# Performance work log

Measured on AMD Instinct MI355X. Metric: run time of the kernel, lower is better.

The kernel has to match this reference:

```python
import jax, jax.numpy as jnp
import numpy as np

B, K, MAX_PER = 128, 3, 48
MAX_TOK = MAX_PER * K  # 144 decode steps
LATENT, HDIM, NMEM = 128, 512, 8
NHEADS, VOCAB = 8, 8000
DH = HDIM // NHEADS
BOS, EOS = 1, 2
ACTIVE_THRESH = 0.01


def setup_inputs() -> dict:
    key = jax.random.key(0)
    ks = jax.random.split(key, 15)
    w = lambda i, sh: jax.random.normal(ks[i], sh, jnp.float32) * 0.05
    return {
        'z_seq': jax.random.normal(ks[0], (B, K, LATENT), jnp.float32),
        'z_weights': jax.random.uniform(ks[1], (B, K), dtype=jnp.float32),
        'W_l2d': w(2, (LATENT, NMEM * HDIM)),
        'token_emb': w(3, (VOCAB, HDIM)),
        'Wq': w(4, (HDIM, HDIM)), 'Wk': w(5, (HDIM, HDIM)),
        'Wv': w(6, (HDIM, HDIM)), 'Wo': w(7, (HDIM, HDIM)),
        'Wcq': w(8, (HDIM, HDIM)), 'Wck': w(9, (HDIM, HDIM)),
        'Wcv': w(10, (HDIM, HDIM)), 'Wco': w(11, (HDIM, HDIM)),
        'W1': w(12, (HDIM, 4 * HDIM)), 'W2': w(13, (4 * HDIM, HDIM)),
        'Wout': w(14, (HDIM, VOCAB)),
    }


def _forward(z_seq, z_weights, W_l2d, token_emb, Wq, Wk, Wv, Wo,
             Wcq, Wck, Wcv, Wco, W1, W2, Wout):
    scale = float(1.0 / np.sqrt(DH))
    ab = jnp.arange(B)
    # weighted_z = z_weights.unsqueeze(-1) * z_seq; memories via latent_to_decoder
    weighted_z = z_weights[..., None] * z_seq                     # [B,K,L]
    memories = (weighted_z.reshape(B * K, LATENT) @ W_l2d).reshape(B, K, NMEM, HDIM)
    active = z_weights > ACTIVE_THRESH                            # [B,K]

    def gated_mem(cur_phr, done):
        i = jnp.minimum(cur_phr, K - 1)
        m = memories[ab, i]                                       # [B,NMEM,HDIM]
        gate = (active[ab, i] & ~done).astype(m.dtype)
        return m * gate[:, None, None]

    def attn_step(x, m, kc, vc, step):
        # x: [B,HDIM] current token hidden; m: gated memories [B,NMEM,HDIM]
        q = (x @ Wq).reshape(B, NHEADS, DH)
        k = (x @ Wk).reshape(B, 1, NHEADS, DH)
        v = (x @ Wv).reshape(B, 1, NHEADS, DH)
        kc = jax.lax.dynamic_update_slice(kc, k, (0, step, 0, 0))
        vc = jax.lax.dynamic_update_slice(vc, v, (0, step, 0, 0))
        s = jnp.einsum('bhd,bthd->bht', q, kc) * scale
        tmask = jnp.arange(MAX_TOK + 1) <= step                   # valid cache slots
        s = jnp.where(tmask[None, None, :], s, -1e30)
        sa = jnp.einsum('bht,bthd->bhd', jax.nn.softmax(s, axis=-1), vc).reshape(B, HDIM)
        x = x + sa @ Wo
        cq = (x @ Wcq).reshape(B, NHEADS, DH)
        ck = (m @ Wck).reshape(B, NMEM, NHEADS, DH)
        cv = (m @ Wcv).reshape(B, NMEM, NHEADS, DH)
        cs = jnp.einsum('bhd,bmhd->bhm', cq, ck) * scale
        ca = jnp.einsum('bhm,bmhd->bhd', jax.nn.softmax(cs, axis=-1), cv).reshape(B, HDIM)
        x = x + ca @ Wco
        x = x + jax.nn.gelu(x @ W1) @ W2
        return x, kc, vc

    kc = jnp.zeros((B, MAX_TOK + 1, NHEADS, DH), jnp.float32)
    vc = jnp.zeros_like(kc)
    done = ~active[:, 0]
    cur_phr = jnp.zeros(B, jnp.int32)
    tip = jnp.zeros(B, jnp.int32)   # tok_in_phr
    pos = jnp.zeros(B, jnp.int32)
    tokens = jnp.zeros((B, MAX_TOK), jnp.int32)
    genm = jnp.zeros((B, MAX_TOK), bool)
    bounds = jnp.zeros((B, K), jnp.int32)
    emb0 = jnp.broadcast_to(token_emb[BOS], (B, HDIM))
    out, kc, vc = attn_step(emb0, gated_mem(cur_phr, done), kc, vc, 0)

    def body(carry, t):
        out, kc, vc, tokens, genm, bounds, cur_phr, tip, pos, done = carry
        logits = out @ Wout
        nxt = jnp.argmax(logits, axis=-1).astype(jnp.int32)
        live = ~done
        tokens = tokens.at[ab, pos].set(jnp.where(live, nxt, 0))
        genm = genm.at[ab, pos].set(live)
        pos = pos + live.astype(jnp.int32)
        tip = tip + live.astype(jnp.int32)
        eos = (nxt == EOS) & (tip >= 1)
        switch = (eos | (tip >= MAX_PER)) & live
        cur_phr = cur_phr + switch.astype(jnp.int32)
        tip = tip * (~switch).astype(jnp.int32)
        sv = switch & (cur_phr < K)
        cp = jnp.minimum(cur_phr, K - 1)
        bounds = bounds.at[ab, cp].set(jnp.where(sv, pos, bounds[ab, cp]))
        done = done | (cur_phr >= K) | (switch & ~active[ab, cp])
        new_out, kc, vc = attn_step(token_emb[nxt], gated_mem(cur_phr, done), kc, vc, t + 1)
        return (new_out, kc, vc, tokens, genm, bounds, cur_phr, tip, pos, done), out

    carry = (out, kc, vc, tokens, genm, bounds, cur_phr, tip, pos, done)
    carry, hiddens = jax.lax.scan(body, carry, jnp.arange(MAX_TOK))
    # tokens, gen_mask, bounds (as in torch _decode) plus per-step hiddens [T,B,H]
    return carry[3], carry[4], carry[5], hiddens


def reference(z_seq, z_weights, W_l2d, token_emb, Wq, Wk, Wv, Wo, Wcq, Wck, Wcv, Wco, W1, W2, Wout):
    return _forward(z_seq, z_weights, W_l2d, token_emb, Wq, Wk, Wv, Wo,
                    Wcq, Wck, Wcv, Wco, W1, W2, Wout)
```

## Files before the change

kernel.cpp:

```cpp
#include <hip/hip_runtime.h>
#include <math.h>

#define NB 128
#define KPH 3
#define MAXPER 48
#define MAXTOK 144
#define LATENT 128
#define HD 512
#define NMEM 8
#define NH 8
#define VOC 8000
#define CT 145
#define NBLK 512
#define SCALE 0.125f

__device__ __forceinline__ float ldsc(const float* p) {
  return __hip_atomic_load(const_cast<float*>(p), __ATOMIC_RELAXED, __HIP_MEMORY_SCOPE_AGENT);
}
__device__ __forceinline__ void stsc(float* p, float v) {
  __hip_atomic_store(p, v, __ATOMIC_RELAXED, __HIP_MEMORY_SCOPE_AGENT);
}
__device__ __forceinline__ int ldsci(const int* p) {
  return __hip_atomic_load(const_cast<int*>(p), __ATOMIC_RELAXED, __HIP_MEMORY_SCOPE_AGENT);
}
__device__ __forceinline__ void stsci(int* p, int v) {
  __hip_atomic_store(p, v, __ATOMIC_RELAXED, __HIP_MEMORY_SCOPE_AGENT);
}

__device__ __forceinline__ void gload_lds(const float* g, float* l) {
  __builtin_amdgcn_global_load_lds(
      (const __attribute__((address_space(1))) unsigned int*)g,
      (__attribute__((address_space(3))) unsigned int*)l, 4, 0, 0);
}


__global__ void k_zero(float* __restrict__ p, int n) {
  int i = blockIdx.x * blockDim.x + threadIdx.x;
  if (i < n) p[i] = 0.0f;
}

__global__ void k_wz(const float* __restrict__ z_seq, const float* __restrict__ zw,
                     float* __restrict__ out) {
  int i = blockIdx.x * blockDim.x + threadIdx.x;
  if (i < NB * KPH * LATENT) out[i] = zw[i >> 7] * z_seq[i];
}

__global__ void k_copy(const float* __restrict__ src, float* __restrict__ dst, int n) {
  int i = blockIdx.x * blockDim.x + threadIdx.x;
  if (i < n) dst[i] = src[i];
}

__global__ __launch_bounds__(256) void k_gemm(
    const float* __restrict__ A, int lda,
    const float* __restrict__ W, int ldw, int K,
    float* __restrict__ out, int ostride)
{
  __shared__ float As[32][36];
  __shared__ float Ws[32][64];
  const int t = threadIdx.x;
  const int c0 = blockIdx.x * 64, b0 = blockIdx.y * 32;
  const int c = t & 63, g = t >> 6;
  float acc[8] = {0,0,0,0,0,0,0,0};
  const int ra = t >> 3, ka = (t & 7) << 2;
  for (int k0 = 0; k0 < K; k0 += 32) {
    const float4 a4 = *reinterpret_cast<const float4*>(A + (size_t)(b0 + ra) * lda + k0 + ka);
    As[ra][ka] = a4.x; As[ra][ka+1] = a4.y; As[ra][ka+2] = a4.z; As[ra][ka+3] = a4.w;
    #pragma unroll
    for (int e = 0; e < 8; e++) {
      int li = t + e * 256;
      Ws[li >> 6][li & 63] = W[(size_t)(k0 + (li >> 6)) * ldw + c0 + (li & 63)];
    }
    __syncthreads();
    #pragma unroll
    for (int kk = 0; kk < 32; kk++) {
      float wv = Ws[kk][c];
      #pragma unroll
      for (int i = 0; i < 8; i++) acc[i] += As[g*8+i][kk] * wv;
    }
    __syncthreads();
  }
  #pragma unroll
  for (int i = 0; i < 8; i++)
    out[(size_t)(b0 + g * 8 + i) * ostride + c0 + c] = acc[i];
}

__global__ void k_init(const float* __restrict__ zw,
                       int* __restrict__ cur, int* __restrict__ tip, int* __restrict__ pos,
                       int* __restrict__ done, float* __restrict__ gf, int* __restrict__ iph,
                       int* __restrict__ nxt0, int* __restrict__ act)
{
  int b = blockIdx.x * blockDim.x + threadIdx.x;
  if (b < NB) {
    int a0 = zw[b*3+0] > 0.01f;
    act[b*3+0] = a0;
    act[b*3+1] = zw[b*3+1] > 0.01f;
    act[b*3+2] = zw[b*3+2] > 0.01f;
    cur[b] = 0; tip[b] = 0; pos[b] = 0; done[b] = !a0;
    gf[b] = a0 ? 1.0f : 0.0f; iph[b] = 0;
    nxt0[b] = 1;
  }
}


struct DecP {
  const float *temb, *Wq, *Wk, *Wv, *Wo, *Wco, *W1, *W2, *Wout;
  const float *MCK, *MCV, *WCAT;
  float *KC, *VC, *XS, *X2, *X3, *X, *Qb, *CQ, *CQ2, *H1, *GP, *PV, *GF;
  int *PI, *CUR, *TIP, *POS, *DONE, *IPH, *NXT0, *ACT;
  float *TOK, *GEN, *BND, *HID;
  unsigned *bar;
};

__device__ __forceinline__ void gsync(unsigned* bar, unsigned epoch) {
  const int t = threadIdx.x, blk = blockIdx.x;
  __syncthreads();
  if (t == 0)
    __hip_atomic_fetch_add(&bar[(blk & 63) * 32], 1u,
                           __ATOMIC_RELAXED, __HIP_MEMORY_SCOPE_AGENT);
  if (blk == 0) {
    if (t < 64) {
      const unsigned tg = epoch * (NBLK / 64);
      while (__hip_atomic_load(&bar[t * 32], __ATOMIC_RELAXED, __HIP_MEMORY_SCOPE_AGENT) < tg)
        __builtin_amdgcn_s_sleep(2);
      if (t < 8)
        __hip_atomic_store(&bar[2048 + t * 32], epoch,
                           __ATOMIC_RELAXED, __HIP_MEMORY_SCOPE_AGENT);
    }
  } else if (t == 0) {
    while (__hip_atomic_load(&bar[2048 + (blk & 7) * 32],
                             __ATOMIC_RELAXED, __HIP_MEMORY_SCOPE_AGENT) < epoch)
      __builtin_amdgcn_s_sleep(8);
  }
  __syncthreads();
}

__global__ __launch_bounds__(256, 2) void k_decode(DecP p) {
  __shared__ float Ws2[2][64][64];
  __shared__ float U[8704];
  __shared__ int   snxt[8];

  const int t = threadIdx.x;
  const int blk = blockIdx.x;
  unsigned ep = 0;

  auto gemm8 = [&](int bx, int by, const float* A, int lda,
                   const float* W, int ldw, int K,
                   const float* R, int rs,
                   float* out, int os, int oo, int dogelu) {
    float (*As2)[8][72] = (float(*)[8][72])U;
    const int c0 = bx * 64, b0 = by * 8;
    const int c = t & 63, g = t >> 6;
    const int ar = t & 7, ak = t >> 3;
    const int nslab = K >> 6;
    float acc0 = 0.f, acc1 = 0.f;
    float res0 = 0.f, res1 = 0.f;
    if (R) {
      res0 = ldsc(R + (size_t)(b0 + g * 2 + 0) * rs + c0 + c);
      res1 = ldsc(R + (size_t)(b0 + g * 2 + 1) * rs + c0 + c);
    }
    float aR0 = ldsc(A + (size_t)(b0 + ar) * lda + ak);
    float aR1 = ldsc(A + (size_t)(b0 + ar) * lda + 32 + ak);
    #pragma unroll
    for (int e = 0; e < 16; e++)
      gload_lds(W + (size_t)(g * 16 + e) * ldw + c0 + c, &Ws2[0][g * 16 + e][0]);
    for (int j = 0; j < nslab; j++) {
      const int cur = j & 1;
      As2[cur][ar][ak] = aR0;
      As2[cur][ar][ak + 32] = aR1;
      __syncthreads();
      if (j + 1 < nslab) {
        aR0 = ldsc(A + (size_t)(b0 + ar) * lda + (j + 1) * 64 + ak);
        aR1 = ldsc(A + (size_t)(b0 + ar) * lda + (j + 1) * 64 + 32 + ak);
        #pragma unroll
        for (int e = 0; e < 16; e++)
          gload_lds(W + (size_t)((j + 1) * 64 + g * 16 + e) * ldw + c0 + c,
                    &Ws2[cur ^ 1][g * 16 + e][0]);
      }
      #pragma unroll
      for (int kk = 0; kk < 64; kk++) {
        float wv = Ws2[cur][kk][c];
        acc0 += As2[cur][g * 2 + 0][kk] * wv;
        acc1 += As2[cur][g * 2 + 1][kk] * wv;
      }
      __syncthreads();
    }
    #pragma unroll
    for (int i = 0; i < 2; i++) {
      float v = (i == 0) ? acc0 : acc1;
      int b = b0 + g * 2 + i;
      v += (i == 0) ? res0 : res1;
      if (dogelu) {
        float x3 = v * v * v;
        v = 0.5f * v * (1.0f + tanhf(0.7978845608028654f * (v + 0.044715f * x3)));
      }
      stsc(out + (size_t)b * os + oo + c0 + c, v);
    }
  };

  auto gemm8g = [&](int bx, int b0, const float* W,
                    float* out, int os, int oo) {
    float (*As2)[8][72] = (float(*)[8][72])U;
    const int c0 = bx * 64;
    const int c = t & 63, g = t >> 6;
    const int ar = t & 7, ak = t >> 3;
    float acc0 = 0.f, acc1 = 0.f;
    const float* Ar = p.temb + (size_t)snxt[ar] * 512;
    float aR0 = Ar[ak];
    float aR1 = Ar[32 + ak];
    #pragma unroll
    for (int e = 0; e < 16; e++)
      gload_lds(W + (size_t)(g * 16 + e) * 512 + c0 + c, &Ws2[0][g * 16 + e][0]);
    for (int j = 0; j < 8; j++) {
      const int cur = j & 1;
      As2[cur][ar][ak] = aR0;
      As2[cur][ar][ak + 32] = aR1;
      __syncthreads();
      if (j + 1 < 8) {
        aR0 = Ar[(j + 1) * 64 + ak];
        aR1 = Ar[(j + 1) * 64 + 32 + ak];
        #pragma unroll
        for (int e = 0; e < 16; e++)
          gload_lds(W + (size_t)((j + 1) * 64 + g * 16 + e) * 512 + c0 + c,
                    &Ws2[cur ^ 1][g * 16 + e][0]);
      }
      #pragma unroll
      for (int kk = 0; kk < 64; kk++) {
        float wv = Ws2[cur][kk][c];
        acc0 += As2[cur][g * 2 + 0][kk] * wv;
        acc1 += As2[cur][g * 2 + 1][kk] * wv;
      }
      __syncthreads();
    }
    #pragma unroll
    for (int i = 0; i < 2; i++) {
      float v = (i == 0) ? acc0 : acc1;
      int b = b0 + g * 2 + i;
      stsc(out + (size_t)b * os + oo + c0 + c, v);
    }
  };

  auto logits_tile = [&](int bx, int by) {
    float (*AsL)[32][72] = (float(*)[32][72])U;
    const int c0 = bx * 64, b0 = by * 32;
    const int c = t & 63, g = t >> 6;
    const int ar = t & 31, akb = (t >> 5) * 8;
    const int cg = t & 15, rg = t >> 4;
    float acc[2][4] = {{0,0,0,0},{0,0,0,0}};
    float aR[8];
    const float* Ab = p.X + (size_t)(b0 + ar) * 512 + akb;
    #pragma unroll
    for (int u = 0; u < 8; u++) aR[u] = ldsc(Ab + u);
    #pragma unroll
    for (int e = 0; e < 16; e++)
      gload_lds(p.Wout + (size_t)(g * 16 + e) * VOC + c0 + c, &Ws2[0][g * 16 + e][0]);
    for (int j = 0; j < 8; j++) {
      const int cur = j & 1;
      #pragma unroll
      for (int u = 0; u < 8; u++) AsL[cur][ar][akb + u] = aR[u];
      __syncthreads();
      if (j + 1 < 8) {
        #pragma unroll
        for (int u = 0; u < 8; u++) aR[u] = ldsc(Ab + (j + 1) * 64 + u);
        #pragma unroll
        for (int e = 0; e < 16; e++)
          gload_lds(p.Wout + (size_t)((j + 1) * 64 + g * 16 + e) * VOC + c0 + c,
                    &Ws2[cur ^ 1][g * 16 + e][0]);
      }
      #pragma unroll
      for (int kk = 0; kk < 64; kk++) {
        float4 w4 = *reinterpret_cast<const float4*>(&Ws2[cur][kk][cg * 4]);
        float a0 = AsL[cur][rg * 2 + 0][kk];
        float a1 = AsL[cur][rg * 2 + 1][kk];
        acc[0][0] += a0 * w4.x; acc[0][1] += a0 * w4.y;
        acc[0][2] += a0 * w4.z; acc[0][3] += a0 * w4.w;
        acc[1][0] += a1 * w4.x; acc[1][1] += a1 * w4.y;
        acc[1][2] += a1 * w4.z; acc[1][3] += a1 * w4.w;
      }
      __syncthreads();
    }
    #pragma unroll
    for (int i = 0; i < 2; i++) {
      float bv = acc[i][0]; int bix = c0 + cg * 4;
      #pragma unroll
      for (int u = 1; u < 4; u++) {
        float v = acc[i][u];
        if (v > bv) { bv = v; bix = c0 + cg * 4 + u; }
      }
      #pragma unroll
      for (int off = 1; off < 16; off <<= 1) {
        float v2 = __shfl_xor(bv, off, 64);
        int   i2 = __shfl_xor(bix, off, 64);
        if (v2 > bv || (v2 == bv && i2 < bix)) { bv = v2; bix = i2; }
      }
      if (cg == 0) {
        stsc(&p.PV[(size_t)(b0 + rg * 2 + i) * 125 + bx], bv);
        stsci(&p.PI[(size_t)(b0 + rg * 2 + i) * 125 + bx], bix);
      }
    }
    __syncthreads();
  };

  auto state_phase = [&](int s, int b0, int desig) {
    const int r = t >> 5, j = t & 31, b = b0 + r;
    const int vOld = (s - 1) & 1, vNew = s & 1;
    if (s > 0) {
      float bv = -INFINITY; int bix = 0x7fffffff;
      for (int i = j; i < 125; i += 32) {
        float v = ldsc(&p.PV[(size_t)b * 125 + i]);
        int  id = ldsci(&p.PI[(size_t)b * 125 + i]);
        if (v > bv || (v == bv && id < bix)) { bv = v; bix = id; }
      }
      #pragma unroll
      for (int off = 16; off; off >>= 1) {
        float v2 = __shfl_xor(bv, off, 64);
        int   i2 = __shfl_xor(bix, off, 64);
        if (v2 > bv || (v2 == bv && i2 < bix)) { bv = v2; bix = i2; }
      }
      if (j == 0) {
        int nxt = bix;
        int dn = ldsci(&p.DONE[vOld*NB+b]); int live = !dn;
        int pp = ldsci(&p.POS[vOld*NB+b]);
        int tp = ldsci(&p.TIP[vOld*NB+b]);
        int cp = ldsci(&p.CUR[vOld*NB+b]);
        if (desig && pp < MAXTOK) {
          p.TOK[(size_t)b*MAXTOK+pp] = live ? (float)nxt : 0.0f;
          p.GEN[(size_t)b*MAXTOK+pp] = live ? 1.0f : 0.0f;
        }
        pp += live; tp += live;
        int eos = (nxt == 2) && (tp >= 1);
        int sw = (eos || (tp >= MAXPER)) && live;
        cp += sw;
        if (sw) tp = 0;
        int cpc = cp < 2 ? cp : 2;
        if (desig && sw && (cp < KPH)) p.BND[(size_t)b*KPH+cpc] = (float)pp;
        dn = dn || (cp >= KPH) || (sw && !p.ACT[b*3+cpc]);
        stsci(&p.CUR[vNew*NB+b], cp);
        stsci(&p.TIP[vNew*NB+b], tp);
        stsci(&p.POS[vNew*NB+b], pp);
        stsci(&p.DONE[vNew*NB+b], dn);
        stsc(&p.GF[vNew*NB+b], (p.ACT[b*3+cpc] && !dn) ? 1.0f : 0.0f);
        stsci(&p.IPH[vNew*NB+b], cpc);
        snxt[r] = nxt;
      }
    } else {
      if (j == 0) snxt[r] = p.NXT0[b];
    }
    __syncthreads();
  };

  for (int s = 0; s < MAXTOK; s++) {
    if (blk < 384) {
      int which = blk >> 7;
      int loc = blk & 127, bx = loc & 7, by = loc >> 3;
      int b0 = by * 8;
      int desig = (which == 0 && bx == 0);
      state_phase(s, b0, desig);
      if (desig) {
        #pragma unroll
        for (int rep = 0; rep < 16; rep++) {
          int idx = t + rep * 256;
          int rr = idx >> 9, cc = idx & 511;
          stsc(&p.XS[(size_t)(b0 + rr) * 1024 + cc],
               p.temb[(size_t)snxt[rr] * 512 + cc]);
        }
      }
      if (which == 0)      gemm8g(bx, b0, p.Wq, p.Qb, 512, 0);
      else if (which == 1) gemm8g(bx, b0, p.Wk, p.KC, CT*512, s*512);
      else                 gemm8g(bx, b0, p.Wv, p.VC, CT*512, s*512);
    }
    gsync(p.bar, ++ep);

    if (blk < 256) {
      float (*aux)[224] = (float(*)[224])U;
      const int T = s + 1;
      int lane = t & 63, w = t >> 6;
      int task = blk * 4 + w, b = task >> 3, h = task & 7;
      float* ql = aux[w];
      float* sc = aux[w] + 64;
      ql[lane] = ldsc(&p.Qb[(size_t)b * 512 + h * 64 + lane]);
      __syncthreads();
      float lmax = -INFINITY;
      for (int s0 = lane; s0 < T; s0 += 64) {
        const float4* kp = reinterpret_cast<const float4*>(p.KC + ((size_t)b * CT + s0) * 512 + h * 64);
        float d = 0.0f;
        #pragma unroll
        for (int e = 0; e < 16; e++) {
          float4 k4 = kp[e];
          d += ql[4*e]*k4.x + ql[4*e+1]*k4.y + ql[4*e+2]*k4.z + ql[4*e+3]*k4.w;
        }
        d *= SCALE;
        sc[s0] = d;
        lmax = fmaxf(lmax, d);
      }
      #pragma unroll
      for (int off = 32; off; off >>= 1) lmax = fmaxf(lmax, __shfl_xor(lmax, off, 64));
      float lsum = 0.0f;
      for (int s0 = lane; s0 < T; s0 += 64) {
        float e = expf(sc[s0] - lmax);
        sc[s0] = e; lsum += e;
      }
      #pragma unroll
      for (int off = 32; off; off >>= 1) lsum += __shfl_xor(lsum, off, 64);
      __syncthreads();
      float inv = 1.0f / lsum;
      float acc = 0.0f;
      const float* vb = p.VC + (size_t)b * CT * 512 + h * 64 + lane;
      #pragma unroll 4
      for (int s0 = 0; s0 < T; s0++) acc += sc[s0] * vb[(size_t)s0 * 512];
      stsc(&p.XS[(size_t)b * 1024 + 512 + h * 64 + lane], acc * inv);
    }
    gsync(p.bar, ++ep);

    if (blk < 128)
      gemm8(blk & 7, blk >> 3, p.XS + 512, 1024, p.Wo, 512, 512, p.XS, 1024, p.X2, 512, 0, 0);
    else if (blk < 256) {
      int l = blk - 128;
      gemm8(l & 7, l >> 3, p.XS, 1024, p.WCAT, 512, 512, nullptr, 0, p.CQ, 512, 0, 0);
    } else if (blk < 384) {
      int l = blk - 256;
      gemm8(l & 7, l >> 3, p.XS + 512, 1024, p.WCAT + (size_t)512*512, 512, 512,
            nullptr, 0, p.CQ2, 512, 0, 0);
    }
    gsync(p.bar, ++ep);

    if (blk < NB) {
      const int b = blk;
      const int vNew = s & 1;
      float* cq  = U;
      float* ca  = U + 512;
      float* scs = U + 1024;
      cq[t]       = ldsc(&p.CQ[(size_t)b * 512 + t])       + ldsc(&p.CQ2[(size_t)b * 512 + t]);
      cq[t + 256] = ldsc(&p.CQ[(size_t)b * 512 + t + 256]) + ldsc(&p.CQ2[(size_t)b * 512 + t + 256]);
      __syncthreads();
      float gate = ldsc(&p.GF[vNew*NB+b]);
      int ip = ldsci(&p.IPH[vNew*NB+b]);
      const float* mk = p.MCK + (size_t)(b * KPH + ip) * NMEM * 512;
      if (t < 64) {
        int h = t >> 3, m = t & 7;
        const float4* kp = reinterpret_cast<const float4*>(mk + m * 512 + h * 64);
        float d = 0.0f;
        #pragma unroll
        for (int e = 0; e < 16; e++) {
          float4 k4 = kp[e];
          d += cq[h*64+4*e]*k4.x + cq[h*64+4*e+1]*k4.y + cq[h*64+4*e+2]*k4.z + cq[h*64+4*e+3]*k4.w;
        }
        scs[t] = d * SCALE * gate;
      }
      __syncthreads();
      const float* mv = p.MCV + (size_t)(b * KPH + ip) * NMEM * 512;
      #pragma unroll
      for (int half = 0; half < 2; half++) {
        int c = t + half * 256;
        int h = c >> 6;
        float mx = scs[h*8];
        #pragma unroll
        for (int m = 1; m < 8; m++) mx = fmaxf(mx, scs[h*8+m]);
        float ee[8]; float sum = 0.0f;
        #pragma unroll
        for (int m = 0; m < 8; m++) { ee[m] = expf(scs[h*8+m] - mx); sum += ee[m]; }
        float a = 0.0f;
        #pragma unroll
        for (int m = 0; m < 8; m++) a += ee[m] * mv[(size_t)m * 512 + c];
        ca[c] = gate * a / sum;
      }
      __syncthreads();
      #pragma unroll
      for (int half = 0; half < 2; half++) {
        int c = t + half * 256;
        float acc = 0.0f;
        const float* wc = p.Wco + c;
        #pragma unroll 8
        for (int k = 0; k < 512; k++) acc += ca[k] * wc[(size_t)k * 512];
        stsc(&p.X3[(size_t)b * 512 + c], acc + ldsc(&p.X2[(size_t)b * 512 + c]));
      }
    }
    gsync(p.bar, ++ep);

    gemm8(blk & 31, blk >> 5, p.X3, 512, p.W1, 2048, 512, nullptr, 0, p.H1, 2048, 0, 1);
    gsync(p.bar, ++ep);

    {
      int ks = blk >> 7, loc = blk & 127;
      gemm8(loc & 7, loc >> 3, p.H1 + ks * 512, 2048,
            p.W2 + (size_t)ks * 512 * 512, 512, 512,
            nullptr, 0, p.GP + (size_t)ks * NB * 512, 512, 0, 0);
    }
    gsync(p.bar, ++ep);

    if (blk < 256) {
      int el = blk * 256 + t;
      float v = ldsc(&p.X3[el])
              + ldsc(&p.GP[el]) + ldsc(&p.GP[NB*512 + el])
              + ldsc(&p.GP[2*NB*512 + el]) + ldsc(&p.GP[3*NB*512 + el]);
      stsc(&p.X[el], v);
      p.HID[(size_t)s * NB * 512 + el] = v;
    }
    gsync(p.bar, ++ep);

    {
      const int x = blk & 7, idx2 = blk >> 3;
      const int ii = idx2 & 15, by = idx2 >> 4;
      const int bx = x + 8 * ii;
      if (bx < 125) logits_tile(bx, by);
    }
    gsync(p.bar, ++ep);
  }

  if (blk < 128 && (blk & 7) == 0) {
    const int b0 = (blk >> 3) * 8;
    state_phase(MAXTOK, b0, 1);
  }
}


extern "C" void kernel_launch(void* const* d_in, const int* in_sizes, int n_in,
                              void* d_out, int out_size, void* d_ws, size_t ws_size,
                              hipStream_t stream)
{
  const float* z_seq = (const float*)d_in[0];
  const float* z_w   = (const float*)d_in[1];
  const float* W_l2d = (const float*)d_in[2];
  const float* temb  = (const float*)d_in[3];
  const float* Wq  = (const float*)d_in[4];
  const float* Wk  = (const float*)d_in[5];
  const float* Wv  = (const float*)d_in[6];
  const float* Wo  = (const float*)d_in[7];
  const float* Wcq = (const float*)d_in[8];
  const float* Wck = (const float*)d_in[9];
  const float* Wcv = (const float*)d_in[10];
  const float* Wco = (const float*)d_in[11];
  const float* W1  = (const float*)d_in[12];
  const float* W2  = (const float*)d_in[13];
  const float* Wout= (const float*)d_in[14];

  float* fw = (float*)d_ws;
  size_t o = 4096;
  auto alloc = [&](size_t n) { float* r = fw + o; o += (n + 63) & ~(size_t)63; return r; };
  float* MCK = alloc((size_t)NB*KPH*NMEM*HD);
  float* MCV = alloc((size_t)NB*KPH*NMEM*HD);
  float* MEM = alloc((size_t)NB*KPH*NMEM*HD);
  float* KC  = alloc((size_t)NB*CT*HD);
  float* VC  = alloc((size_t)NB*CT*HD);
  float* XS  = alloc((size_t)NB*1024);
  float* X2  = alloc((size_t)NB*HD);
  float* X3  = alloc((size_t)NB*HD);
  float* X   = alloc((size_t)NB*HD);
  float* Qb  = alloc((size_t)NB*HD);
  float* CQ  = alloc((size_t)NB*HD);
  float* H1  = alloc((size_t)NB*4*HD);
  float* WZ  = alloc((size_t)NB*KPH*LATENT);
  float* PV  = alloc((size_t)NB*125);
  float* GF  = alloc(2*NB);
  int* ib = (int*)alloc(0);
  size_t io = 0;
  auto ialloc = [&](size_t n) { int* r = ib + io; io += (n + 63) & ~(size_t)63; return r; };
  int* PI   = ialloc((size_t)NB*125);
  int* CUR  = ialloc(2*NB);
  int* TIP  = ialloc(2*NB);
  int* POS  = ialloc(2*NB);
  int* DONE = ialloc(2*NB);
  int* IPH  = ialloc(2*NB);
  int* NXT0 = ialloc(NB);
  int* ACT  = ialloc(NB*KPH);

  float* WCAT = MEM;
  float* GP   = MEM + (size_t)1024*512;
  float* CQ2  = GP  + (size_t)4*NB*HD;

  float* out_f = (float*)d_out;
  float* TOK  = out_f;
  float* GEN  = out_f + NB*MAXTOK;
  float* BND  = out_f + 2*NB*MAXTOK;
  float* HID  = out_f + 2*NB*MAXTOK + NB*KPH;

  k_zero<<<16, 256, 0, stream>>>(fw, 4096);
  int nz = 2*NB*MAXTOK + NB*KPH;
  k_zero<<<(nz + 255)/256, 256, 0, stream>>>(out_f, nz);
  k_wz<<<(NB*KPH*LATENT + 255)/256, 256, 0, stream>>>(z_seq, z_w, WZ);
  k_gemm<<<dim3(64,12),256,0,stream>>>(WZ, 128, W_l2d, 4096, 128, MEM, 4096);
  k_gemm<<<dim3(8,96),256,0,stream>>>(MEM, 512, Wck, 512, 512, MCK, 512);
  k_gemm<<<dim3(8,96),256,0,stream>>>(MEM, 512, Wcv, 512, 512, MCV, 512);
  k_gemm<<<dim3(8,16),256,0,stream>>>(Wo, 512, Wcq, 512, 512, WCAT + (size_t)512*512, 512);
  k_copy<<<(512*512 + 255)/256, 256, 0, stream>>>(Wcq, WCAT, 512*512);
  k_init<<<1,128,0,stream>>>(z_w, CUR, TIP, POS, DONE, GF, IPH, NXT0, ACT);

  DecP prm;
  prm.temb = temb; prm.Wq = Wq; prm.Wk = Wk; prm.Wv = Wv; prm.Wo = Wo;
  prm.Wco = Wco; prm.W1 = W1; prm.W2 = W2; prm.Wout = Wout;
  prm.MCK = MCK; prm.MCV = MCV; prm.WCAT = WCAT;
  prm.KC = KC; prm.VC = VC; prm.XS = XS; prm.X2 = X2; prm.X3 = X3; prm.X = X;
  prm.Qb = Qb; prm.CQ = CQ; prm.CQ2 = CQ2; prm.H1 = H1; prm.GP = GP;
  prm.PV = PV; prm.GF = GF;
  prm.PI = PI; prm.CUR = CUR; prm.TIP = TIP; prm.POS = POS; prm.DONE = DONE;
  prm.IPH = IPH; prm.NXT0 = NXT0; prm.ACT = ACT;
  prm.TOK = TOK; prm.GEN = GEN; prm.BND = BND; prm.HID = HID;
  prm.bar = (unsigned*)d_ws;

  k_decode<<<dim3(NBLK), dim3(256), 0, stream>>>(prm);
}
```

Measured before the change: 30.28 ms.

## Widen GEMM tiles to 128 columns and cut active blocks per phase

The persistent decode kernel's GEMM helpers now compute 128-column tiles with 2x2 register blocking over 32-wide K slabs, replacing 64-column tiles. The logits GEMM uses 128x32 tiles with 4x4 blocking, which halves the number of argmax partials per row from 125 to 63. Each phase now uses fewer blocks (192 or 256 instead of 384 or 512). The aim is more reuse per loaded weight and fewer partial results, at the cost of less parallelism per phase and more barrier steps per slab.

```diff
diff --git a/kernel.cpp b/kernel.cpp
--- a/kernel.cpp
+++ b/kernel.cpp
@@ -143,158 +143,173 @@
   const int blk = blockIdx.x;
   unsigned ep = 0;
 
-  auto gemm8 = [&](int bx, int by, const float* A, int lda,
+  const int wv = t >> 6, lc = t & 63;
+
+  auto gemm4 = [&](int bx, int by, const float* A, int lda,
                    const float* W, int ldw, int K,
                    const float* R, int rs,
                    float* out, int os, int oo, int dogelu) {
-    float (*As2)[8][72] = (float(*)[8][72])U;
-    const int c0 = bx * 64, b0 = by * 8;
-    const int c = t & 63, g = t >> 6;
-    const int ar = t & 7, ak = t >> 3;
-    const int nslab = K >> 6;
-    float acc0 = 0.f, acc1 = 0.f;
-    float res0 = 0.f, res1 = 0.f;
+    float (*Ws)[32][128] = (float(*)[32][128])Ws2;
+    float (*As)[8][36]   = (float(*)[8][36])U;
+    const int c0 = bx * 128, b0 = by * 8;
+    const int cg = t & 63, rg = t >> 6;
+    const int sr = t >> 5, sk = t & 31;
+    const int nslab = K >> 5;
+    float acc[2][2] = {{0.f,0.f},{0.f,0.f}};
+    float res[2][2] = {{0.f,0.f},{0.f,0.f}};
     if (R) {
-      res0 = ldsc(R + (size_t)(b0 + g * 2 + 0) * rs + c0 + c);
-      res1 = ldsc(R + (size_t)(b0 + g * 2 + 1) * rs + c0 + c);
-    }
-    float aR0 = ldsc(A + (size_t)(b0 + ar) * lda + ak);
-    float aR1 = ldsc(A + (size_t)(b0 + ar) * lda + 32 + ak);
+      #pragma unroll
+      for (int i = 0; i < 2; i++)
+        #pragma unroll
+        for (int jj = 0; jj < 2; jj++)
+          res[i][jj] = ldsc(R + (size_t)(b0 + rg * 2 + i) * rs + c0 + cg * 2 + jj);
+    }
+    float aS = ldsc(A + (size_t)(b0 + sr) * lda + sk);
     #pragma unroll
     for (int e = 0; e < 16; e++)
-      gload_lds(W + (size_t)(g * 16 + e) * ldw + c0 + c, &Ws2[0][g * 16 + e][0]);
+      gload_lds(W + (size_t)(wv * 8 + (e >> 1)) * ldw + c0 + (e & 1) * 64 + lc,
+                &Ws[0][wv * 8 + (e >> 1)][(e & 1) * 64]);
     for (int j = 0; j < nslab; j++) {
       const int cur = j & 1;
-      As2[cur][ar][ak] = aR0;
-      As2[cur][ar][ak + 32] = aR1;
+      As[cur][sr][sk] = aS;
       __syncthreads();
       if (j + 1 < nslab) {
-        aR0 = ldsc(A + (size_t)(b0 + ar) * lda + (j + 1) * 64 + ak);
-        aR1 = ldsc(A + (size_t)(b0 + ar) * lda + (j + 1) * 64 + 32 + ak);
+        aS = ldsc(A + (size_t)(b0 + sr) * lda + (j + 1) * 32 + sk);
         #pragma unroll
         for (int e = 0; e < 16; e++)
-          gload_lds(W + (size_t)((j + 1) * 64 + g * 16 + e) * ldw + c0 + c,
-                    &Ws2[cur ^ 1][g * 16 + e][0]);
-      }
-      #pragma unroll
-      for (int kk = 0; kk < 64; kk++) {
-        float wv = Ws2[cur][kk][c];
-        acc0 += As2[cur][g * 2 + 0][kk] * wv;
-        acc1 += As2[cur][g * 2 + 1][kk] * wv;
+          gload_lds(W + (size_t)((j + 1) * 32 + wv * 8 + (e >> 1)) * ldw + c0 + (e & 1) * 64 + lc,
+                    &Ws[cur ^ 1][wv * 8 + (e >> 1)][(e & 1) * 64]);
+      }
+      #pragma unroll
+      for (int kk = 0; kk < 32; kk++) {
+        float2 w2 = *reinterpret_cast<const float2*>(&Ws[cur][kk][cg * 2]);
+        float a0 = As[cur][rg * 2 + 0][kk];
+        float a1 = As[cur][rg * 2 + 1][kk];
+        acc[0][0] += a0 * w2.x; acc[0][1] += a0 * w2.y;
+        acc[1][0] += a1 * w2.x; acc[1][1] += a1 * w2.y;
       }
       __syncthreads();
     }
     #pragma unroll
     for (int i = 0; i < 2; i++) {
-      float v = (i == 0) ? acc0 : acc1;
-      int b = b0 + g * 2 + i;
-      v += (i == 0) ? res0 : res1;
-      if (dogelu) {
-        float x3 = v * v * v;
-        v = 0.5f * v * (1.0f + tanhf(0.7978845608028654f * (v + 0.044715f * x3)));
-      }
-      stsc(out + (size_t)b * os + oo + c0 + c, v);
+      #pragma unroll
+      for (int jj = 0; jj < 2; jj++) {
+        float v = acc[i][jj] + res[i][jj];
+        if (dogelu) {
+          float x3 = v * v * v;
+          v = 0.5f * v * (1.0f + tanhf(0.7978845608028654f * (v + 0.044715f * x3)));
+        }
+        stsc(out + (size_t)(b0 + rg * 2 + i) * os + oo + c0 + cg * 2 + jj, v);
+      }
     }
   };
 
-  auto gemm8g = [&](int bx, int b0, const float* W,
+  auto gemm4g = [&](int bx, int b0, const float* W,
                     float* out, int os, int oo) {
-    float (*As2)[8][72] = (float(*)[8][72])U;
-    const int c0 = bx * 64;
-    const int c = t & 63, g = t >> 6;
-    const int ar = t & 7, ak = t >> 3;
-    float acc0 = 0.f, acc1 = 0.f;
-    const float* Ar = p.temb + (size_t)snxt[ar] * 512;
-    float aR0 = Ar[ak];
-    float aR1 = Ar[32 + ak];
+    float (*Ws)[32][128] = (float(*)[32][128])Ws2;
+    float (*As)[8][36]   = (float(*)[8][36])U;
+    const int c0 = bx * 128;
+    const int cg = t & 63, rg = t >> 6;
+    const int sr = t >> 5, sk = t & 31;
+    float acc[2][2] = {{0.f,0.f},{0.f,0.f}};
+    const float* Ar = p.temb + (size_t)snxt[sr] * 512;
+    float aS = Ar[sk];
     #pragma unroll
     for (int e = 0; e < 16; e++)
-      gload_lds(W + (size_t)(g * 16 + e) * 512 + c0 + c, &Ws2[0][g * 16 + e][0]);
-    for (int j = 0; j < 8; j++) {
+      gload_lds(W + (size_t)(wv * 8 + (e >> 1)) * 512 + c0 + (e & 1) * 64 + lc,
+                &Ws[0][wv * 8 + (e >> 1)][(e & 1) * 64]);
+    for (int j = 0; j < 16; j++) {
       const int cur = j & 1;
-      As2[cur][ar][ak] = aR0;
-      As2[cur][ar][ak + 32] = aR1;
-      __syncthreads();
-      if (j + 1 < 8) {
-        aR0 = Ar[(j + 1) * 64 + ak];
-        aR1 = Ar[(j + 1) * 64 + 32 + ak];
+      As[cur][sr][sk] = aS;
+      __syncthreads();
+      if (j + 1 < 16) {
+        aS = Ar[(j + 1) * 32 + sk];
         #pragma unroll
         for (int e = 0; e < 16; e++)
-          gload_lds(W + (size_t)((j + 1) * 64 + g * 16 + e) * 512 + c0 + c,
-                    &Ws2[cur ^ 1][g * 16 + e][0]);
-      }
-      #pragma unroll
-      for (int kk = 0; kk < 64; kk++) {
-        float wv = Ws2[cur][kk][c];
-        acc0 += As2[cur][g * 2 + 0][kk] * wv;
-        acc1 += As2[cur][g * 2 + 1][kk] * wv;
-      }
-      __syncthreads();
-    }
-    #pragma unroll
-    for (int i = 0; i < 2; i++) {
-      float v = (i == 0) ? acc0 : acc1;
-      int b = b0 + g * 2 + i;
-      stsc(out + (size_t)b * os + oo + c0 + c, v);
-    }
+          gload_lds(W + (size_t)((j + 1) * 32 + wv * 8 + (e >> 1)) * 512 + c0 + (e & 1) * 64 + lc,
+                    &Ws[cur ^ 1][wv * 8 + (e >> 1)][(e & 1) * 64]);
+      }
+      #pragma unroll
+      for (int kk = 0; kk < 32; kk++) {
+        float2 w2 = *reinterpret_cast<const float2*>(&Ws[cur][kk][cg * 2]);
+        float a0 = As[cur][rg * 2 + 0][kk];
+        float a1 = As[cur][rg * 2 + 1][kk];
+        acc[0][0] += a0 * w2.x; acc[0][1] += a0 * w2.y;
+        acc[1][0] += a1 * w2.x; acc[1][1] += a1 * w2.y;
+      }
+      __syncthreads();
+    }
+    #pragma unroll
+    for (int i = 0; i < 2; i++)
+      #pragma unroll
+      for (int jj = 0; jj < 2; jj++)
+        stsc(out + (size_t)(b0 + rg * 2 + i) * os + oo + c0 + cg * 2 + jj, acc[i][jj]);
   };
 
-  auto logits_tile = [&](int bx, int by) {
-    float (*AsL)[32][72] = (float(*)[32][72])U;
-    const int c0 = bx * 64, b0 = by * 32;
-    const int c = t & 63, g = t >> 6;
-    const int ar = t & 31, akb = (t >> 5) * 8;
-    const int cg = t & 15, rg = t >> 4;
-    float acc[2][4] = {{0,0,0,0},{0,0,0,0}};
-    float aR[8];
-    const float* Ab = p.X + (size_t)(b0 + ar) * 512 + akb;
-    #pragma unroll
-    for (int u = 0; u < 8; u++) aR[u] = ldsc(Ab + u);
-    #pragma unroll
-    for (int e = 0; e < 16; e++)
-      gload_lds(p.Wout + (size_t)(g * 16 + e) * VOC + c0 + c, &Ws2[0][g * 16 + e][0]);
-    for (int j = 0; j < 8; j++) {
+  auto logits128 = [&](int ct, int rt) {
+    float (*Ws)[32][128] = (float(*)[32][128])Ws2;
+    float (*As)[32][36]  = (float(*)[32][36])U;
+    const int c0 = ct * 128, b0 = rt * 32;
+    const int cg = t & 31, rg = t >> 5;
+    const int sr = t & 31, sk = (t >> 5) * 4;
+    float acc[4][4] = {{0,0,0,0},{0,0,0,0},{0,0,0,0},{0,0,0,0}};
+    float aR[4];
+    const float* Ab = p.X + (size_t)(b0 + sr) * 512 + sk;
+    #pragma unroll
+    for (int u = 0; u < 4; u++) aR[u] = ldsc(Ab + u);
+    #pragma unroll
+    for (int e = 0; e < 16; e++) {
+      int col = c0 + (e & 1) * 64 + lc;
+      if (col >= VOC) col = VOC - 1;
+      gload_lds(p.Wout + (size_t)(wv * 8 + (e >> 1)) * VOC + col,
+                &Ws[0][wv * 8 + (e >> 1)][(e & 1) * 64]);
+    }
+    for (int j = 0; j < 16; j++) {
       const int cur = j & 1;
       #pragma unroll
-      for (int u = 0; u < 8; u++) AsL[cur][ar][akb + u] = aR[u];
-      __syncthreads();
-      if (j + 1 < 8) {
-        #pragma unroll
-        for (int u = 0; u < 8; u++) aR[u] = ldsc(Ab + (j + 1) * 64 + u);
-        #pragma unroll
-        for (int e = 0; e < 16; e++)
-          gload_lds(p.Wout + (size_t)((j + 1) * 64 + g * 16 + e) * VOC + c0 + c,
-                    &Ws2[cur ^ 1][g * 16 + e][0]);
-      }
-      #pragma unroll
-      for (int kk = 0; kk < 64; kk++) {
-        float4 w4 = *reinterpret_cast<const float4*>(&Ws2[cur][kk][cg * 4]);
-        float a0 = AsL[cur][rg * 2 + 0][kk];
-        float a1 = AsL[cur][rg * 2 + 1][kk];
-        acc[0][0] += a0 * w4.x; acc[0][1] += a0 * w4.y;
-        acc[0][2] += a0 * w4.z; acc[0][3] += a0 * w4.w;
-        acc[1][0] += a1 * w4.x; acc[1][1] += a1 * w4.y;
-        acc[1][2] += a1 * w4.z; acc[1][3] += a1 * w4.w;
-      }
-      __syncthreads();
-    }
-    #pragma unroll
-    for (int i = 0; i < 2; i++) {
-      float bv = acc[i][0]; int bix = c0 + cg * 4;
-      #pragma unroll
-      for (int u = 1; u < 4; u++) {
-        float v = acc[i][u];
-        if (v > bv) { bv = v; bix = c0 + cg * 4 + u; }
-      }
-      #pragma unroll
-      for (int off = 1; off < 16; off <<= 1) {
+      for (int u = 0; u < 4; u++) As[cur][sr][sk + u] = aR[u];
+      __syncthreads();
+      if (j + 1 < 16) {
+        #pragma unroll
+        for (int u = 0; u < 4; u++) aR[u] = ldsc(Ab + (j + 1) * 32 + u);
+        #pragma unroll
+        for (int e = 0; e < 16; e++) {
+          int col = c0 + (e & 1) * 64 + lc;
+          if (col >= VOC) col = VOC - 1;
+          gload_lds(p.Wout + (size_t)((j + 1) * 32 + wv * 8 + (e >> 1)) * VOC + col,
+                    &Ws[cur ^ 1][wv * 8 + (e >> 1)][(e & 1) * 64]);
+        }
+      }
+      #pragma unroll
+      for (int kk = 0; kk < 32; kk++) {
+        float4 w4 = *reinterpret_cast<const float4*>(&Ws[cur][kk][cg * 4]);
+        #pragma unroll
+        for (int i = 0; i < 4; i++) {
+          float a = As[cur][rg * 4 + i][kk];
+          acc[i][0] += a * w4.x; acc[i][1] += a * w4.y;
+          acc[i][2] += a * w4.z; acc[i][3] += a * w4.w;
+        }
+      }
+      __syncthreads();
+    }
+    #pragma unroll
+    for (int i = 0; i < 4; i++) {
+      float bv = -INFINITY; int bix = 0x7fffffff;
+      #pragma unroll
+      for (int u = 0; u < 4; u++) {
+        int c = c0 + cg * 4 + u;
+        float v = (c < VOC) ? acc[i][u] : -INFINITY;
+        if (v > bv) { bv = v; bix = c; }
+      }
+      #pragma unroll
+      for (int off = 16; off; off >>= 1) {
         float v2 = __shfl_xor(bv, off, 64);
         int   i2 = __shfl_xor(bix, off, 64);
         if (v2 > bv || (v2 == bv && i2 < bix)) { bv = v2; bix = i2; }
       }
       if (cg == 0) {
-        stsc(&p.PV[(size_t)(b0 + rg * 2 + i) * 125 + bx], bv);
-        stsci(&p.PI[(size_t)(b0 + rg * 2 + i) * 125 + bx], bix);
+        stsc(&p.PV[(size_t)(b0 + rg * 4 + i) * 64 + ct], bv);
+        stsci(&p.PI[(size_t)(b0 + rg * 4 + i) * 64 + ct], bix);
       }
     }
     __syncthreads();
@@ -305,9 +320,9 @@
     const int vOld = (s - 1) & 1, vNew = s & 1;
     if (s > 0) {
       float bv = -INFINITY; int bix = 0x7fffffff;
-      for (int i = j; i < 125; i += 32) {
-        float v = ldsc(&p.PV[(size_t)b * 125 + i]);
-        int  id = ldsci(&p.PI[(size_t)b * 125 + i]);
+      for (int i = j; i < 63; i += 32) {
+        float v = ldsc(&p.PV[(size_t)b * 64 + i]);
+        int  id = ldsci(&p.PI[(size_t)b * 64 + i]);
         if (v > bv || (v == bv && id < bix)) { bv = v; bix = id; }
       }
       #pragma unroll
@@ -349,9 +364,9 @@
   };
 
   for (int s = 0; s < MAXTOK; s++) {
-    if (blk < 384) {
-      int which = blk >> 7;
-      int loc = blk & 127, bx = loc & 7, by = loc >> 3;
+    if (blk < 192) {
+      int which = blk >> 6;
+      int loc = blk & 63, bx = loc & 3, by = loc >> 2;
       int b0 = by * 8;
       int desig = (which == 0 && bx == 0);
       state_phase(s, b0, desig);
@@ -364,9 +379,9 @@
                p.temb[(size_t)snxt[rr] * 512 + cc]);
         }
       }
-      if (which == 0)      gemm8g(bx, b0, p.Wq, p.Qb, 512, 0);
-      else if (which == 1) gemm8g(bx, b0, p.Wk, p.KC, CT*512, s*512);
-      else                 gemm8g(bx, b0, p.Wv, p.VC, CT*512, s*512);
+      if (which == 0)      gemm4g(bx, b0, p.Wq, p.Qb, 512, 0);
+      else if (which == 1) gemm4g(bx, b0, p.Wk, p.KC, CT*512, s*512);
+      else                 gemm4g(bx, b0, p.Wv, p.VC, CT*512, s*512);
     }
     gsync(p.bar, ++ep);
 
@@ -411,14 +426,14 @@
     }
     gsync(p.bar, ++ep);
 
-    if (blk < 128)
-      gemm8(blk & 7, blk >> 3, p.XS + 512, 1024, p.Wo, 512, 512, p.XS, 1024, p.X2, 512, 0, 0);
-    else if (blk < 256) {
+    if (blk < 64)
+      gemm4(blk & 3, blk >> 2, p.XS + 512, 1024, p.Wo, 512, 512, p.XS, 1024, p.X2, 512, 0, 0);
+    else if (blk < 128) {
+      int l = blk - 64;
+      gemm4(l & 3, l >> 2, p.XS, 1024, p.WCAT, 512, 512, nullptr, 0, p.CQ, 512, 0, 0);
+    } else if (blk < 192) {
       int l = blk - 128;
-      gemm8(l & 7, l >> 3, p.XS, 1024, p.WCAT, 512, 512, nullptr, 0, p.CQ, 512, 0, 0);
-    } else if (blk < 384) {
-      int l = blk - 256;
-      gemm8(l & 7, l >> 3, p.XS + 512, 1024, p.WCAT + (size_t)512*512, 512, 512,
+      gemm4(l & 3, l >> 2, p.XS + 512, 1024, p.WCAT + (size_t)512*512, 512, 512,
             nullptr, 0, p.CQ2, 512, 0, 0);
     }
     gsync(p.bar, ++ep);
@@ -476,12 +491,13 @@
     }
     gsync(p.bar, ++ep);
 
-    gemm8(blk & 31, blk >> 5, p.X3, 512, p.W1, 2048, 512, nullptr, 0, p.H1, 2048, 0, 1);
-    gsync(p.bar, ++ep);
-
-    {
-      int ks = blk >> 7, loc = blk & 127;
-      gemm8(loc & 7, loc >> 3, p.H1 + ks * 512, 2048,
+    if (blk < 256)
+      gemm4(blk & 15, blk >> 4, p.X3, 512, p.W1, 2048, 512, nullptr, 0, p.H1, 2048, 0, 1);
+    gsync(p.bar, ++ep);
+
+    if (blk < 256) {
+      int ks = blk >> 6, loc = blk & 63;
+      gemm4(loc & 3, loc >> 2, p.H1 + ks * 512, 2048,
             p.W2 + (size_t)ks * 512 * 512, 512, 512,
             nullptr, 0, p.GP + (size_t)ks * NB * 512, 512, 0, 0);
     }
@@ -497,11 +513,10 @@
     }
     gsync(p.bar, ++ep);
 
-    {
-      const int x = blk & 7, idx2 = blk >> 3;
-      const int ii = idx2 & 15, by = idx2 >> 4;
-      const int bx = x + 8 * ii;
-      if (bx < 125) logits_tile(bx, by);
+    if (blk < 256) {
+      const int ct = (blk & 7) + 8 * ((blk >> 3) & 7);
+      const int rt = blk >> 6;
+      if (ct < 63) logits128(ct, rt);
     }
     gsync(p.bar, ++ep);
   }
@@ -549,12 +564,12 @@
   float* CQ  = alloc((size_t)NB*HD);
   float* H1  = alloc((size_t)NB*4*HD);
   float* WZ  = alloc((size_t)NB*KPH*LATENT);
-  float* PV  = alloc((size_t)NB*125);
+  float* PV  = alloc((size_t)NB*64);
   float* GF  = alloc(2*NB);
   int* ib = (int*)alloc(0);
   size_t io = 0;
   auto ialloc = [&](size_t n) { int* r = ib + io; io += (n + 63) & ~(size_t)63; return r; };
-  int* PI   = ialloc((size_t)NB*125);
+  int* PI   = ialloc((size_t)NB*64);
   int* CUR  = ialloc(2*NB);
   int* TIP  = ialloc(2*NB);
   int* POS  = ialloc(2*NB);
```

Result: slower. 66.88 ms (+120.9%).

## Switch decode GEMM tiles from 8 to 16 batch rows with float4 LDS reads

Applied to the files above, without the earlier changes.

Each GEMM block now computes a 16-row by 64-column output tile, with every thread producing four adjacent columns from vectorized float4 weight reads out of shared memory. This halves how many blocks stream each weight tile, cutting redundant weight traffic in the QKV, Wo, cross-query, W1 and W2 projections. The state and argmax phases are remapped to 16 rows per block, using 16 lanes per row. The trade-off is that half as many blocks are active in these phases, and each block does twice the work between grid-wide barriers.

```diff
diff --git a/kernel.cpp b/kernel.cpp
--- a/kernel.cpp
+++ b/kernel.cpp
@@ -137,40 +137,45 @@
 __global__ __launch_bounds__(256, 2) void k_decode(DecP p) {
   __shared__ float Ws2[2][64][64];
   __shared__ float U[8704];
-  __shared__ int   snxt[8];
+  __shared__ int   snxt[16];
 
   const int t = threadIdx.x;
   const int blk = blockIdx.x;
   unsigned ep = 0;
 
-  auto gemm8 = [&](int bx, int by, const float* A, int lda,
-                   const float* W, int ldw, int K,
-                   const float* R, int rs,
-                   float* out, int os, int oo, int dogelu) {
-    float (*As2)[8][72] = (float(*)[8][72])U;
-    const int c0 = bx * 64, b0 = by * 8;
+  const int wv = t >> 6;
+  (void)wv;
+
+  auto gemm16 = [&](int bx, int by, const float* A, int lda,
+                    const float* W, int ldw, int K,
+                    const float* R, int rs,
+                    float* out, int os, int oo, int dogelu) {
+    float (*As2)[16][72] = (float(*)[16][72])U;
+    const int c0 = bx * 64, b0 = by * 16;
     const int c = t & 63, g = t >> 6;
-    const int ar = t & 7, ak = t >> 3;
+    const int cg = t & 15, rg = t >> 4;
+    const int sr = t & 15, sk = (t >> 4) * 4;
     const int nslab = K >> 6;
-    float acc0 = 0.f, acc1 = 0.f;
-    float res0 = 0.f, res1 = 0.f;
+    float acc[4] = {0,0,0,0};
+    float res[4] = {0,0,0,0};
     if (R) {
-      res0 = ldsc(R + (size_t)(b0 + g * 2 + 0) * rs + c0 + c);
-      res1 = ldsc(R + (size_t)(b0 + g * 2 + 1) * rs + c0 + c);
-    }
-    float aR0 = ldsc(A + (size_t)(b0 + ar) * lda + ak);
-    float aR1 = ldsc(A + (size_t)(b0 + ar) * lda + 32 + ak);
+      #pragma unroll
+      for (int u = 0; u < 4; u++)
+        res[u] = ldsc(R + (size_t)(b0 + rg) * rs + c0 + cg * 4 + u);
+    }
+    const float* Ab = A + (size_t)(b0 + sr) * lda + sk;
+    float aP0 = ldsc(Ab + 0), aP1 = ldsc(Ab + 1), aP2 = ldsc(Ab + 2), aP3 = ldsc(Ab + 3);
     #pragma unroll
     for (int e = 0; e < 16; e++)
       gload_lds(W + (size_t)(g * 16 + e) * ldw + c0 + c, &Ws2[0][g * 16 + e][0]);
     for (int j = 0; j < nslab; j++) {
       const int cur = j & 1;
-      As2[cur][ar][ak] = aR0;
-      As2[cur][ar][ak + 32] = aR1;
+      As2[cur][sr][sk + 0] = aP0; As2[cur][sr][sk + 1] = aP1;
+      As2[cur][sr][sk + 2] = aP2; As2[cur][sr][sk + 3] = aP3;
       __syncthreads();
       if (j + 1 < nslab) {
-        aR0 = ldsc(A + (size_t)(b0 + ar) * lda + (j + 1) * 64 + ak);
-        aR1 = ldsc(A + (size_t)(b0 + ar) * lda + (j + 1) * 64 + 32 + ak);
+        const float* Ab2 = Ab + (j + 1) * 64;
+        aP0 = ldsc(Ab2 + 0); aP1 = ldsc(Ab2 + 1); aP2 = ldsc(Ab2 + 2); aP3 = ldsc(Ab2 + 3);
         #pragma unroll
         for (int e = 0; e < 16; e++)
           gload_lds(W + (size_t)((j + 1) * 64 + g * 16 + e) * ldw + c0 + c,
@@ -178,46 +183,45 @@
       }
       #pragma unroll
       for (int kk = 0; kk < 64; kk++) {
-        float wv = Ws2[cur][kk][c];
-        acc0 += As2[cur][g * 2 + 0][kk] * wv;
-        acc1 += As2[cur][g * 2 + 1][kk] * wv;
-      }
-      __syncthreads();
-    }
-    #pragma unroll
-    for (int i = 0; i < 2; i++) {
-      float v = (i == 0) ? acc0 : acc1;
-      int b = b0 + g * 2 + i;
-      v += (i == 0) ? res0 : res1;
+        float4 w4 = *reinterpret_cast<const float4*>(&Ws2[cur][kk][cg * 4]);
+        float a = As2[cur][rg][kk];
+        acc[0] += a * w4.x; acc[1] += a * w4.y;
+        acc[2] += a * w4.z; acc[3] += a * w4.w;
+      }
+      __syncthreads();
+    }
+    #pragma unroll
+    for (int u = 0; u < 4; u++) {
+      float v = acc[u] + res[u];
       if (dogelu) {
         float x3 = v * v * v;
         v = 0.5f * v * (1.0f + tanhf(0.7978845608028654f * (v + 0.044715f * x3)));
       }
-      stsc(out + (size_t)b * os + oo + c0 + c, v);
+      stsc(out + (size_t)(b0 + rg) * os + oo + c0 + cg * 4 + u, v);
     }
   };
 
-  auto gemm8g = [&](int bx, int b0, const float* W,
-                    float* out, int os, int oo) {
-    float (*As2)[8][72] = (float(*)[8][72])U;
+  auto gemm16g = [&](int bx, int b0, const float* W,
+                     float* out, int os, int oo) {
+    float (*As2)[16][72] = (float(*)[16][72])U;
     const int c0 = bx * 64;
     const int c = t & 63, g = t >> 6;
-    const int ar = t & 7, ak = t >> 3;
-    float acc0 = 0.f, acc1 = 0.f;
-    const float* Ar = p.temb + (size_t)snxt[ar] * 512;
-    float aR0 = Ar[ak];
-    float aR1 = Ar[32 + ak];
+    const int cg = t & 15, rg = t >> 4;
+    const int sr = t & 15, sk = (t >> 4) * 4;
+    float acc[4] = {0,0,0,0};
+    const float* Ar = p.temb + (size_t)snxt[sr] * 512;
+    float aP0 = Ar[sk + 0], aP1 = Ar[sk + 1], aP2 = Ar[sk + 2], aP3 = Ar[sk + 3];
     #pragma unroll
     for (int e = 0; e < 16; e++)
       gload_lds(W + (size_t)(g * 16 + e) * 512 + c0 + c, &Ws2[0][g * 16 + e][0]);
     for (int j = 0; j < 8; j++) {
       const int cur = j & 1;
-      As2[cur][ar][ak] = aR0;
-      As2[cur][ar][ak + 32] = aR1;
+      As2[cur][sr][sk + 0] = aP0; As2[cur][sr][sk + 1] = aP1;
+      As2[cur][sr][sk + 2] = aP2; As2[cur][sr][sk + 3] = aP3;
       __syncthreads();
       if (j + 1 < 8) {
-        aR0 = Ar[(j + 1) * 64 + ak];
-        aR1 = Ar[(j + 1) * 64 + 32 + ak];
+        const float* Ar2 = Ar + (j + 1) * 64 + sk;
+        aP0 = Ar2[0]; aP1 = Ar2[1]; aP2 = Ar2[2]; aP3 = Ar2[3];
         #pragma unroll
         for (int e = 0; e < 16; e++)
           gload_lds(W + (size_t)((j + 1) * 64 + g * 16 + e) * 512 + c0 + c,
@@ -225,18 +229,16 @@
       }
       #pragma unroll
       for (int kk = 0; kk < 64; kk++) {
-        float wv = Ws2[cur][kk][c];
-        acc0 += As2[cur][g * 2 + 0][kk] * wv;
-        acc1 += As2[cur][g * 2 + 1][kk] * wv;
-      }
-      __syncthreads();
-    }
-    #pragma unroll
-    for (int i = 0; i < 2; i++) {
-      float v = (i == 0) ? acc0 : acc1;
-      int b = b0 + g * 2 + i;
-      stsc(out + (size_t)b * os + oo + c0 + c, v);
-    }
+        float4 w4 = *reinterpret_cast<const float4*>(&Ws2[cur][kk][cg * 4]);
+        float a = As2[cur][rg][kk];
+        acc[0] += a * w4.x; acc[1] += a * w4.y;
+        acc[2] += a * w4.z; acc[3] += a * w4.w;
+      }
+      __syncthreads();
+    }
+    #pragma unroll
+    for (int u = 0; u < 4; u++)
+      stsc(out + (size_t)(b0 + rg) * os + oo + c0 + cg * 4 + u, acc[u]);
   };
 
   auto logits_tile = [&](int bx, int by) {
@@ -301,17 +303,17 @@
   };
 
   auto state_phase = [&](int s, int b0, int desig) {
-    const int r = t >> 5, j = t & 31, b = b0 + r;
+    const int r = t >> 4, j = t & 15, b = b0 + r;
     const int vOld = (s - 1) & 1, vNew = s & 1;
     if (s > 0) {
       float bv = -INFINITY; int bix = 0x7fffffff;
-      for (int i = j; i < 125; i += 32) {
+      for (int i = j; i < 125; i += 16) {
         float v = ldsc(&p.PV[(size_t)b * 125 + i]);
         int  id = ldsci(&p.PI[(size_t)b * 125 + i]);
         if (v > bv || (v == bv && id < bix)) { bv = v; bix = id; }
       }
       #pragma unroll
-      for (int off = 16; off; off >>= 1) {
+      for (int off = 8; off; off >>= 1) {
         float v2 = __shfl_xor(bv, off, 64);
         int   i2 = __shfl_xor(bix, off, 64);
         if (v2 > bv || (v2 == bv && i2 < bix)) { bv = v2; bix = i2; }
@@ -349,24 +351,24 @@
   };
 
   for (int s = 0; s < MAXTOK; s++) {
-    if (blk < 384) {
-      int which = blk >> 7;
-      int loc = blk & 127, bx = loc & 7, by = loc >> 3;
-      int b0 = by * 8;
+    if (blk < 192) {
+      int which = blk >> 6;
+      int loc = blk & 63, bx = loc & 7, by = loc >> 3;
+      int b0 = by * 16;
       int desig = (which == 0 && bx == 0);
       state_phase(s, b0, desig);
       if (desig) {
         #pragma unroll
-        for (int rep = 0; rep < 16; rep++) {
+        for (int rep = 0; rep < 32; rep++) {
           int idx = t + rep * 256;
           int rr = idx >> 9, cc = idx & 511;
           stsc(&p.XS[(size_t)(b0 + rr) * 1024 + cc],
                p.temb[(size_t)snxt[rr] * 512 + cc]);
         }
       }
-      if (which == 0)      gemm8g(bx, b0, p.Wq, p.Qb, 512, 0);
-      else if (which == 1) gemm8g(bx, b0, p.Wk, p.KC, CT*512, s*512);
-      else                 gemm8g(bx, b0, p.Wv, p.VC, CT*512, s*512);
+      if (which == 0)      gemm16g(bx, b0, p.Wq, p.Qb, 512, 0);
+      else if (which == 1) gemm16g(bx, b0, p.Wk, p.KC, CT*512, s*512);
+      else                 gemm16g(bx, b0, p.Wv, p.VC, CT*512, s*512);
     }
     gsync(p.bar, ++ep);
 
@@ -411,15 +413,15 @@
     }
     gsync(p.bar, ++ep);
 
-    if (blk < 128)
-      gemm8(blk & 7, blk >> 3, p.XS + 512, 1024, p.Wo, 512, 512, p.XS, 1024, p.X2, 512, 0, 0);
-    else if (blk < 256) {
+    if (blk < 64)
+      gemm16(blk & 7, blk >> 3, p.XS + 512, 1024, p.Wo, 512, 512, p.XS, 1024, p.X2, 512, 0, 0);
+    else if (blk < 128) {
+      int l = blk - 64;
+      gemm16(l & 7, l >> 3, p.XS, 1024, p.WCAT, 512, 512, nullptr, 0, p.CQ, 512, 0, 0);
+    } else if (blk < 192) {
       int l = blk - 128;
-      gemm8(l & 7, l >> 3, p.XS, 1024, p.WCAT, 512, 512, nullptr, 0, p.CQ, 512, 0, 0);
-    } else if (blk < 384) {
-      int l = blk - 256;
-      gemm8(l & 7, l >> 3, p.XS + 512, 1024, p.WCAT + (size_t)512*512, 512, 512,
-            nullptr, 0, p.CQ2, 512, 0, 0);
+      gemm16(l & 7, l >> 3, p.XS + 512, 1024, p.WCAT + (size_t)512*512, 512, 512,
+             nullptr, 0, p.CQ2, 512, 0, 0);
     }
     gsync(p.bar, ++ep);
 
@@ -476,14 +478,15 @@
     }
     gsync(p.bar, ++ep);
 
-    gemm8(blk & 31, blk >> 5, p.X3, 512, p.W1, 2048, 512, nullptr, 0, p.H1, 2048, 0, 1);
-    gsync(p.bar, ++ep);
-
-    {
-      int ks = blk >> 7, loc = blk & 127;
-      gemm8(loc & 7, loc >> 3, p.H1 + ks * 512, 2048,
-            p.W2 + (size_t)ks * 512 * 512, 512, 512,
-            nullptr, 0, p.GP + (size_t)ks * NB * 512, 512, 0, 0);
+    if (blk < 256)
+      gemm16(blk & 31, blk >> 5, p.X3, 512, p.W1, 2048, 512, nullptr, 0, p.H1, 2048, 0, 1);
+    gsync(p.bar, ++ep);
+
+    if (blk < 256) {
+      int ks = blk >> 6, loc = blk & 63;
+      gemm16(loc & 7, loc >> 3, p.H1 + ks * 512, 2048,
+             p.W2 + (size_t)ks * 512 * 512, 512, 512,
+             nullptr, 0, p.GP + (size_t)ks * NB * 512, 512, 0, 0);
     }
     gsync(p.bar, ++ep);
 
@@ -506,8 +509,8 @@
     gsync(p.bar, ++ep);
   }
 
-  if (blk < 128 && (blk & 7) == 0) {
-    const int b0 = (blk >> 3) * 8;
+  if (blk < 128 && (blk & 15) == 0) {
+    const int b0 = (blk >> 4) * 16;
     state_phase(MAXTOK, b0, 1);
   }
 }
```

New measurement: 27.75 ms. 1.09x faster.
